# Performance work log

Measured on AMD Instinct MI355X. Metric: run time of the kernel, lower is better.

Reference implementation:

```python
import jax, jax.numpy as jnp
import numpy as np

D_MODEL = 512
NHEAD = 8
DIM = D_MODEL // NHEAD
EPS_ATT = 1e-6
EPS_LN = 1e-5


def layer_norm(x, gamma, beta):
    mu = jnp.mean(x, axis=-1, keepdims=True)
    var = jnp.mean(jnp.square(x - mu), axis=-1, keepdims=True)
    return (x - mu) * jax.lax.rsqrt(var + EPS_LN) * gamma + beta


def setup_inputs() -> dict:
    key = jax.random.key(0)
    ks = jax.random.split(key, 12)
    B, L = 4, 4096
    s = 1.0 / np.sqrt(D_MODEL)
    inp = {
        "q": jax.random.normal(ks[0], (B, L, D_MODEL), jnp.float32),
        "k": jax.random.normal(ks[1], (B, L, D_MODEL), jnp.float32),
        "v": jax.random.normal(ks[2], (B, L, D_MODEL), jnp.float32),
        # weights stored [in, out] so application is x @ W (== torch Linear with W.T)
        "Wq": jax.random.normal(ks[3], (D_MODEL, D_MODEL), jnp.float32) * s,
        "Wk": jax.random.normal(ks[4], (D_MODEL, D_MODEL), jnp.float32) * s,
        "Wv": jax.random.normal(ks[5], (D_MODEL, D_MODEL), jnp.float32) * s,
        "Wm": jax.random.normal(ks[6], (D_MODEL, D_MODEL), jnp.float32) * s,
        "W1": jax.random.normal(ks[7], (D_MODEL, 4 * D_MODEL), jnp.float32) * s,
        "W2": jax.random.normal(ks[8], (4 * D_MODEL, D_MODEL), jnp.float32) * (0.5 * s),
        "g1": jnp.ones((D_MODEL,), jnp.float32),
        "b1": jnp.zeros((D_MODEL,), jnp.float32),
        "g2": jnp.ones((D_MODEL,), jnp.float32),
        "b2": jnp.zeros((D_MODEL,), jnp.float32),
    }
    return inp


def reference(q, k, v, Wq, Wk, Wv, Wm, W1, W2, g1, b1, g2, b2):
    B, L, _ = q.shape
    S = k.shape[1]
    # projections -> [B, L, H, D]
    Qp = (q @ Wq).reshape(B, L, NHEAD, DIM)
    Kp = (k @ Wk).reshape(B, S, NHEAD, DIM)
    Vp = (v @ Wv).reshape(B, S, NHEAD, DIM)
    # elu+1 feature map linear attention
    Q = jax.nn.elu(Qp) + 1.0
    K = jax.nn.elu(Kp) + 1.0
    Vn = Vp / S
    KV = jnp.einsum('nshd,nshv->nhdv', K, Vn)          # [B,H,D,D]
    Z = 1.0 / (jnp.einsum('nlhd,nhd->nlh', Q, K.sum(axis=1)) + EPS_ATT)
    msg = jnp.einsum('nlhd,nhdv,nlh->nlhv', Q, KV, Z) * S  # [B,L,H,D]
    # merge + residual + norm1
    msg = msg.reshape(B, L, D_MODEL) @ Wm
    msg = layer_norm(msg + q, g1, b1)
    # FFN; note original adds mlp output to q (not norm1 output)
    ffn = jax.nn.relu(msg @ W1) @ W2
    out = layer_norm(q + ffn, g2, b2)
    return out
```

## Files before the change

### kernel.cpp

```cpp
#include <hip/hip_runtime.h>

typedef unsigned short u16;
typedef unsigned int u32;

typedef __bf16 bf16x8 __attribute__((ext_vector_type(8)));
typedef float f32x4 __attribute__((ext_vector_type(4)));

#define EPI_BF16 0
#define EPI_ELU1 1
#define EPI_RELU 2
#define EPI_ADDRES_F32 3
#define EPI_PROJ3 4

__device__ __forceinline__ float bf2f(u16 x) {
    u32 u = ((u32)x) << 16;
    return __uint_as_float(u);
}
__device__ __forceinline__ u16 f2bf(float f) {
    u32 u = __float_as_uint(f);
    u32 r = (u + 0x7FFFu + ((u >> 16) & 1u)) >> 16;
    return (u16)r;
}

__device__ __forceinline__ void gload_lds16(const u16* g, u16* l) {
    __builtin_amdgcn_global_load_lds(
        (const __attribute__((address_space(1))) u32*)g,
        (__attribute__((address_space(3))) u32*)l, 16, 0, 0);
}

__global__ __launch_bounds__(256) void prep_k(
    const float* __restrict__ q, const float* __restrict__ k,
    const float* __restrict__ v,
    const float* __restrict__ Wq, const float* __restrict__ Wk,
    const float* __restrict__ Wv, const float* __restrict__ Wm,
    const float* __restrict__ W1, const float* __restrict__ W2,
    u16* __restrict__ qkv_out, u16* __restrict__ wt4_out,
    u16* __restrict__ wt2_out)
{
    int bid = blockIdx.x;
    if (bid < 24576) {
        int w = bid >> 13;
        const float* in = (w == 0) ? q : (w == 1) ? k : v;
        int i = ((bid & 8191) * 256 + threadIdx.x) * 4;
        float4 f = *(const float4*)(in + i);
        ushort4 o;
        o.x = f2bf(f.x); o.y = f2bf(f.y); o.z = f2bf(f.z); o.w = f2bf(f.w);
        *(ushort4*)(qkv_out + (long)w * 8388608 + i) = o;
    } else if (bid < 28672) {
        int idx = (bid - 24576) * 256 + threadIdx.x;
        int w = idx >> 18, local = idx & 262143;
        const float* in = (w == 0) ? Wq : (w == 1) ? Wk : (w == 2) ? Wv : Wm;
        int c = local >> 9, r = local & 511;
        wt4_out[idx] = f2bf(in[r * 512 + c]);
    } else {
        int idx = (bid - 28672) * 256 + threadIdx.x;
        if (idx < 1048576) {
            int c = idx / 512, r = idx % 512;
            wt2_out[idx] = f2bf(W1[(long)r * 2048 + c]);
        } else {
            int local = idx - 1048576;
            int c = local / 2048, r = local % 2048;
            wt2_out[idx] = f2bf(W2[(long)r * 512 + c]);
        }
    }
}

__global__ __launch_bounds__(256) void gemm_bt(
    const u16* __restrict__ A, const u16* __restrict__ Bt,
    void* __restrict__ C, const float* __restrict__ Res,
    int M, int N, int K, int epi)
{
    __shared__ __align__(16) u16 As[2][4096];
    __shared__ __align__(16) u16 Bs[2][4096];

    int t = threadIdx.x;
    int gx = gridDim.x;
    int nwg = gx * gridDim.y;
    int bid = blockIdx.y * gx + blockIdx.x;
    if ((nwg & 7) == 0) {
        int cpx = nwg >> 3;
        bid = (bid & 7) * cpx + (bid >> 3);
    }
    int m0 = (bid / gx) * 128, n0 = (bid % gx) * 128;

    int third = 0;
    if (epi == EPI_PROJ3) {
        third = n0 >> 9;
        A += (long)third * 8388608;
    }

    int wave = t >> 6, lane = t & 63;
    int wm = (wave >> 1) * 64, wn = (wave & 1) * 64;
    int lrow = lane & 15, lk8 = (lane >> 4) * 8;

    f32x4 acc[4][4] = {};

    int srow = wave * 16 + (lane >> 2);
    int scol = (lane & 3) * 8;
    const u16* pA0 = A + (long)(m0 + srow) * K + scol;
    const u16* pB0 = Bt + (long)(n0 + srow) * K + scol;
    const long s64 = (long)64 * K;

    int nt = K >> 5;
    int cur = 0;

    {
        u16* a = As[0] + wave * 512;
        u16* b = Bs[0] + wave * 512;
        gload_lds16(pA0, a);
        gload_lds16(pA0 + s64, a + 2048);
        gload_lds16(pB0, b);
        gload_lds16(pB0 + s64, b + 2048);
    }
    __builtin_amdgcn_s_waitcnt(0);
    __syncthreads();

    for (int kt = 0; kt < nt; ++kt) {
        if (kt + 1 < nt) {
            int k0 = (kt + 1) << 5;
            u16* a = As[cur ^ 1] + wave * 512;
            u16* b = Bs[cur ^ 1] + wave * 512;
            gload_lds16(pA0 + k0, a);
            gload_lds16(pA0 + s64 + k0, a + 2048);
            gload_lds16(pB0 + k0, b);
            gload_lds16(pB0 + s64 + k0, b + 2048);
        }

        const u16* As_c = As[cur];
        const u16* Bs_c = Bs[cur];
        bf16x8 af[4], bfr[4];
#pragma unroll
        for (int mi = 0; mi < 4; mi++)
            af[mi] = *(const bf16x8*)(As_c + (wm + mi * 16 + lrow) * 32 + lk8);
#pragma unroll
        for (int ni = 0; ni < 4; ni++)
            bfr[ni] = *(const bf16x8*)(Bs_c + (wn + ni * 16 + lrow) * 32 + lk8);
#pragma unroll
        for (int mi = 0; mi < 4; mi++)
#pragma unroll
            for (int ni = 0; ni < 4; ni++)
                acc[mi][ni] = __builtin_amdgcn_mfma_f32_16x16x32_bf16(
                    af[mi], bfr[ni], acc[mi][ni], 0, 0, 0);

        if (kt + 1 < nt) {
            __builtin_amdgcn_s_waitcnt(0);
            __syncthreads();
            cur ^= 1;
        }
    }

    int rq = (lane >> 4) * 4;
    int colb = n0 + wn + (lane & 15);
#pragma unroll
    for (int mi = 0; mi < 4; mi++) {
#pragma unroll
        for (int ni = 0; ni < 4; ni++) {
#pragma unroll
            for (int r = 0; r < 4; r++) {
                int row = m0 + wm + mi * 16 + rq + r;
                int col = colb + ni * 16;
                float v0 = acc[mi][ni][r];
                if (epi == EPI_PROJ3) {
                    u16* Cb = (u16*)C + (long)third * 8388608;
                    long idx = (long)row * 512 + (col - (third << 9));
                    float v = (third < 2)
                                  ? (v0 > 0.f ? v0 + 1.f : __expf(v0))
                                  : v0;
                    Cb[idx] = f2bf(v);
                } else {
                    long idx = (long)row * N + col;
                    if (epi == EPI_ELU1) {
                        float v = v0 > 0.f ? v0 + 1.f : __expf(v0);
                        ((u16*)C)[idx] = f2bf(v);
                    } else if (epi == EPI_RELU) {
                        ((u16*)C)[idx] = f2bf(v0 > 0.f ? v0 : 0.f);
                    } else if (epi == EPI_ADDRES_F32) {
                        ((float*)C)[idx] = v0 + Res[idx];
                    } else {
                        ((u16*)C)[idx] = f2bf(v0);
                    }
                }
            }
        }
    }
}

__global__ __launch_bounds__(256) void gemm_bt64(
    const u16* __restrict__ A, const u16* __restrict__ Bt,
    void* __restrict__ C, const float* __restrict__ Res,
    int M, int N, int K, int epi)
{
    __shared__ __align__(16) u16 As[2][8192];
    __shared__ __align__(16) u16 Bs[2][8192];

    int t = threadIdx.x;
    int gx = gridDim.x;
    int nwg = gx * gridDim.y;
    int bid = blockIdx.y * gx + blockIdx.x;
    if ((nwg & 7) == 0) {
        int cpx = nwg >> 3;
        bid = (bid & 7) * cpx + (bid >> 3);
    }
    int m0 = (bid / gx) * 128, n0 = (bid % gx) * 128;

    int wave = t >> 6, lane = t & 63;
    int wm = (wave >> 1) * 64, wn = (wave & 1) * 64;
    int lrow = lane & 15, lk8 = (lane >> 4) * 8;

    f32x4 acc[4][4] = {};

    int srow = wave * 16 + (lane >> 2);
    int scol = (lane & 3) * 8;
    const u16* pA0 = A + (long)(m0 + srow) * K + scol;
    const u16* pB0 = Bt + (long)(n0 + srow) * K + scol;
    const long s64 = (long)64 * K;

    int nt = K >> 6;
    int cur = 0;

    {
        u16* a = As[0] + wave * 512;
        u16* b = Bs[0] + wave * 512;
#pragma unroll
        for (int kk = 0; kk < 2; kk++) {
            gload_lds16(pA0 + kk * 32, a + kk * 4096);
            gload_lds16(pA0 + s64 + kk * 32, a + kk * 4096 + 2048);
            gload_lds16(pB0 + kk * 32, b + kk * 4096);
            gload_lds16(pB0 + s64 + kk * 32, b + kk * 4096 + 2048);
        }
    }
    __builtin_amdgcn_s_waitcnt(0);
    __syncthreads();

    for (int kt = 0; kt < nt; ++kt) {
        if (kt + 1 < nt) {
            int k0 = (kt + 1) << 6;
            u16* a = As[cur ^ 1] + wave * 512;
            u16* b = Bs[cur ^ 1] + wave * 512;
#pragma unroll
            for (int kk = 0; kk < 2; kk++) {
                gload_lds16(pA0 + k0 + kk * 32, a + kk * 4096);
                gload_lds16(pA0 + s64 + k0 + kk * 32, a + kk * 4096 + 2048);
                gload_lds16(pB0 + k0 + kk * 32, b + kk * 4096);
                gload_lds16(pB0 + s64 + k0 + kk * 32, b + kk * 4096 + 2048);
            }
        }

#pragma unroll
        for (int kk = 0; kk < 2; kk++) {
            const u16* As_c = As[cur] + kk * 4096;
            const u16* Bs_c = Bs[cur] + kk * 4096;
            bf16x8 af[4], bfr[4];
#pragma unroll
            for (int mi = 0; mi < 4; mi++)
                af[mi] = *(const bf16x8*)(As_c + (wm + mi * 16 + lrow) * 32 + lk8);
#pragma unroll
            for (int ni = 0; ni < 4; ni++)
                bfr[ni] = *(const bf16x8*)(Bs_c + (wn + ni * 16 + lrow) * 32 + lk8);
#pragma unroll
            for (int mi = 0; mi < 4; mi++)
#pragma unroll
                for (int ni = 0; ni < 4; ni++)
                    acc[mi][ni] = __builtin_amdgcn_mfma_f32_16x16x32_bf16(
                        af[mi], bfr[ni], acc[mi][ni], 0, 0, 0);
        }

        if (kt + 1 < nt) {
            __builtin_amdgcn_s_waitcnt(0);
            __syncthreads();
            cur ^= 1;
        }
    }

    int rq = (lane >> 4) * 4;
    int colb = n0 + wn + (lane & 15);
#pragma unroll
    for (int mi = 0; mi < 4; mi++) {
#pragma unroll
        for (int ni = 0; ni < 4; ni++) {
#pragma unroll
            for (int r = 0; r < 4; r++) {
                int row = m0 + wm + mi * 16 + rq + r;
                int col = colb + ni * 16;
                long idx = (long)row * N + col;
                float v0 = acc[mi][ni][r];
                if (epi == EPI_ELU1) {
                    float v = v0 > 0.f ? v0 + 1.f : __expf(v0);
                    ((u16*)C)[idx] = f2bf(v);
                } else if (epi == EPI_RELU) {
                    ((u16*)C)[idx] = f2bf(v0 > 0.f ? v0 : 0.f);
                } else if (epi == EPI_ADDRES_F32) {
                    ((float*)C)[idx] = v0 + Res[idx];
                } else {
                    ((u16*)C)[idx] = f2bf(v0);
                }
            }
        }
    }
}

__global__ __launch_bounds__(256) void kv_part(
    const u16* __restrict__ Kf, const u16* __restrict__ Vf,
    float* __restrict__ Part, float* __restrict__ KsPart)
{
    __shared__ __align__(16) u16 sKt[64 * 72];
    __shared__ __align__(16) u16 sVt[64 * 72];
    int bh = blockIdx.x;
    int b = bh >> 3, h = bh & 7;
    int t = threadIdx.x;
    int wave = t >> 6, lane = t & 63;
    int dblk = (wave >> 1) * 32, vblk = (wave & 1) * 32;
    int lrow = lane & 15, lk8 = (lane >> 4) * 8;

    f32x4 acc[2][2] = {};
    float ks = 0.f;

    int srow = t >> 2, c16 = (t & 3) * 16;

    for (int st = 0; st < 2; ++st) {
        int s0 = blockIdx.y * 128 + st * 64;
        {
            long g = ((long)b * 4096 + s0 + srow) * 512 + h * 64 + c16;
            uint4 k0 = *(const uint4*)(Kf + g);
            uint4 k1 = *(const uint4*)(Kf + g + 8);
            uint4 v0 = *(const uint4*)(Vf + g);
            uint4 v1 = *(const uint4*)(Vf + g + 8);
            u32 kw[8] = {k0.x, k0.y, k0.z, k0.w, k1.x, k1.y, k1.z, k1.w};
            u32 vw[8] = {v0.x, v0.y, v0.z, v0.w, v1.x, v1.y, v1.z, v1.w};
            if (st) __syncthreads();
#pragma unroll
            for (int j = 0; j < 16; j++) {
                u16 kv_ = (u16)(kw[j >> 1] >> ((j & 1) * 16));
                u16 vv_ = (u16)(vw[j >> 1] >> ((j & 1) * 16));
                sKt[(c16 + j) * 72 + srow] = kv_;
                sVt[(c16 + j) * 72 + srow] = vv_;
            }
        }
        __syncthreads();

#pragma unroll
        for (int ksb = 0; ksb < 2; ++ksb) {
            int ko = ksb * 32 + lk8;
            bf16x8 a0 = *(const bf16x8*)(sKt + (dblk + lrow) * 72 + ko);
            bf16x8 a1 = *(const bf16x8*)(sKt + (dblk + 16 + lrow) * 72 + ko);
            bf16x8 b0 = *(const bf16x8*)(sVt + (vblk + lrow) * 72 + ko);
            bf16x8 b1 = *(const bf16x8*)(sVt + (vblk + 16 + lrow) * 72 + ko);
            acc[0][0] = __builtin_amdgcn_mfma_f32_16x16x32_bf16(a0, b0, acc[0][0], 0, 0, 0);
            acc[0][1] = __builtin_amdgcn_mfma_f32_16x16x32_bf16(a0, b1, acc[0][1], 0, 0, 0);
            acc[1][0] = __builtin_amdgcn_mfma_f32_16x16x32_bf16(a1, b0, acc[1][0], 0, 0, 0);
            acc[1][1] = __builtin_amdgcn_mfma_f32_16x16x32_bf16(a1, b1, acc[1][1], 0, 0, 0);
        }

        if (t < 64) {
            const u32* rowp = (const u32*)(sKt + t * 72);
#pragma unroll
            for (int c = 0; c < 32; c++) {
                u32 w = rowp[c];
                ks += bf2f((u16)w) + bf2f((u16)(w >> 16));
            }
        }
    }

    int rq = (lane >> 4) * 4;
    float* pp = Part + ((long)bh * 32 + blockIdx.y) * 4096;
#pragma unroll
    for (int ti = 0; ti < 2; ti++)
#pragma unroll
        for (int tj = 0; tj < 2; tj++)
#pragma unroll
            for (int r = 0; r < 4; r++) {
                int d = dblk + ti * 16 + rq + r;
                int vcol = vblk + tj * 16 + (lane & 15);
                pp[d * 64 + vcol] = acc[ti][tj][r];
            }
    if (t < 64) KsPart[((bh * 32) + blockIdx.y) * 64 + t] = ks;
}

__global__ __launch_bounds__(256) void kv_reduce(
    const float* __restrict__ Part, const float* __restrict__ KsPart,
    float* __restrict__ KV, float* __restrict__ Ksum)
{
    int i = blockIdx.x * 256 + threadIdx.x;
    if (i < 131072) {
        int bh = i >> 12, dv = i & 4095;
        const float* p = Part + (long)bh * 32 * 4096 + dv;
        float s = 0.f;
#pragma unroll 8
        for (int sp = 0; sp < 32; sp++) s += p[(long)sp * 4096];
        KV[i] = s;
    } else if (i < 133120) {
        int j = i - 131072;
        int bh = j >> 6, d = j & 63;
        const float* p = KsPart + bh * 32 * 64 + d;
        float s = 0.f;
#pragma unroll 8
        for (int sp = 0; sp < 32; sp++) s += p[sp * 64];
        Ksum[j] = s;
    }
}

__global__ __launch_bounds__(256) void msg_k(
    const u16* __restrict__ Q, const float* __restrict__ KV,
    const float* __restrict__ Ksum, u16* __restrict__ Msg)
{
    __shared__ float sKVt[64 * 68];
    __shared__ float sQ[64 * 68];
    __shared__ float sKs[64];
    __shared__ float sZ[64];

    int bh = blockIdx.x;
    int b = bh >> 3, h = bh & 7;
    int l0 = blockIdx.y * 64;
    int t = threadIdx.x, wave = t >> 6, lane = t & 63;

    {
        const float* src = KV + (long)bh * 4096 + t * 16;
        int d = t >> 2;
        int v0 = (t & 3) * 16;
        float4 a0 = *(const float4*)(src);
        float4 a1 = *(const float4*)(src + 4);
        float4 a2 = *(const float4*)(src + 8);
        float4 a3 = *(const float4*)(src + 12);
        float tmp[16] = {a0.x, a0.y, a0.z, a0.w, a1.x, a1.y, a1.z, a1.w,
                         a2.x, a2.y, a2.z, a2.w, a3.x, a3.y, a3.z, a3.w};
#pragma unroll
        for (int j = 0; j < 16; j++) sKVt[(v0 + j) * 68 + d] = tmp[j];
    }
    {
        int row = t >> 2, c = (t & 3) * 16;
        const u16* src = Q + ((long)b * 4096 + l0 + row) * 512 + h * 64 + c;
        uint4 q0 = *(const uint4*)(src);
        uint4 q1 = *(const uint4*)(src + 8);
        float* dq = sQ + row * 68 + c;
        u32 qw[8] = {q0.x, q0.y, q0.z, q0.w, q1.x, q1.y, q1.z, q1.w};
#pragma unroll
        for (int j = 0; j < 8; j++) {
            dq[2 * j]     = __uint_as_float(qw[j] << 16);
            dq[2 * j + 1] = __uint_as_float(qw[j] & 0xFFFF0000u);
        }
    }
    if (t < 64) sKs[t] = Ksum[bh * 64 + t];
    __syncthreads();

    float kv[64];
    {
        const float* kr = sKVt + lane * 68;
#pragma unroll
        for (int j = 0; j < 16; j++) {
            float4 x = *(const float4*)(kr + 4 * j);
            kv[4 * j]     = x.x; kv[4 * j + 1] = x.y;
            kv[4 * j + 2] = x.z; kv[4 * j + 3] = x.w;
        }
    }
    if (t < 64) {
        const float* qr = sQ + t * 68;
        float zp = 0.f;
#pragma unroll
        for (int d = 0; d < 64; d++) zp += qr[d] * sKs[d];
        sZ[t] = 1.f / (zp + 1e-6f);
    }
    __syncthreads();

    const long obase = ((long)b * 4096 + l0) * 512 + h * 64 + lane;
    int lbase = wave * 16;
#pragma unroll 4
    for (int i = 0; i < 16; i++) {
        int ll = lbase + i;
        const float* qr = sQ + ll * 68;
        float a0 = 0.f, a1 = 0.f, a2 = 0.f, a3 = 0.f;
#pragma unroll
        for (int db = 0; db < 16; db++) {
            float4 q4 = *(const float4*)(qr + 4 * db);
            a0 += q4.x * kv[4 * db];
            a1 += q4.y * kv[4 * db + 1];
            a2 += q4.z * kv[4 * db + 2];
            a3 += q4.w * kv[4 * db + 3];
        }
        float acc = (a0 + a1) + (a2 + a3);
        Msg[obase + (long)ll * 512] = f2bf(acc * sZ[ll]);
    }
}

__global__ __launch_bounds__(256) void ln_k(
    const float* __restrict__ X, const float* __restrict__ g,
    const float* __restrict__ bta, u16* __restrict__ OutB,
    float* __restrict__ OutF, int out_f32)
{
    int wave = threadIdx.x >> 6, lane = threadIdx.x & 63;
    long row = (long)blockIdx.x * 4 + wave;
    const float* x = X + row * 512 + lane * 8;
    float4 a = *(const float4*)(x);
    float4 c = *(const float4*)(x + 4);
    float s = (a.x + a.y) + (a.z + a.w) + (c.x + c.y) + (c.z + c.w);
    float sq = a.x * a.x + a.y * a.y + a.z * a.z + a.w * a.w +
               c.x * c.x + c.y * c.y + c.z * c.z + c.w * c.w;
#pragma unroll
    for (int off = 32; off > 0; off >>= 1) {
        s += __shfl_xor(s, off, 64);
        sq += __shfl_xor(sq, off, 64);
    }
    float mu = s * (1.f / 512.f);
    float var = sq * (1.f / 512.f) - mu * mu;
    float rstd = rsqrtf(var + 1e-5f);
    float4 g0 = *(const float4*)(g + lane * 8);
    float4 g1 = *(const float4*)(g + lane * 8 + 4);
    float4 b0 = *(const float4*)(bta + lane * 8);
    float4 b1 = *(const float4*)(bta + lane * 8 + 4);
    float y0 = (a.x - mu) * rstd * g0.x + b0.x;
    float y1 = (a.y - mu) * rstd * g0.y + b0.y;
    float y2 = (a.z - mu) * rstd * g0.z + b0.z;
    float y3 = (a.w - mu) * rstd * g0.w + b0.w;
    float y4 = (c.x - mu) * rstd * g1.x + b1.x;
    float y5 = (c.y - mu) * rstd * g1.y + b1.y;
    float y6 = (c.z - mu) * rstd * g1.z + b1.z;
    float y7 = (c.w - mu) * rstd * g1.w + b1.w;
    if (out_f32) {
        float* o = OutF + row * 512 + lane * 8;
        *(float4*)(o) = make_float4(y0, y1, y2, y3);
        *(float4*)(o + 4) = make_float4(y4, y5, y6, y7);
    } else {
        u32 w0 = (u32)f2bf(y0) | ((u32)f2bf(y1) << 16);
        u32 w1 = (u32)f2bf(y2) | ((u32)f2bf(y3) << 16);
        u32 w2 = (u32)f2bf(y4) | ((u32)f2bf(y5) << 16);
        u32 w3 = (u32)f2bf(y6) | ((u32)f2bf(y7) << 16);
        uint4 o = {w0, w1, w2, w3};
        *(uint4*)(OutB + row * 512 + lane * 8) = o;
    }
}

extern "C" void kernel_launch(void* const* d_in, const int* in_sizes, int n_in,
                              void* d_out, int out_size, void* d_ws, size_t ws_size,
                              hipStream_t stream) {
    const float* q  = (const float*)d_in[0];
    const float* k  = (const float*)d_in[1];
    const float* v  = (const float*)d_in[2];
    const float* Wq = (const float*)d_in[3];
    const float* Wk = (const float*)d_in[4];
    const float* Wv = (const float*)d_in[5];
    const float* Wm = (const float*)d_in[6];
    const float* W1 = (const float*)d_in[7];
    const float* W2 = (const float*)d_in[8];
    const float* g1 = (const float*)d_in[9];
    const float* b1 = (const float*)d_in[10];
    const float* g2 = (const float*)d_in[11];
    const float* b2 = (const float*)d_in[12];

    char* ws = (char*)d_ws;
    u16* WTq = (u16*)(ws + 0);
    u16* W1T = (u16*)(ws + 2097152);
    u16* qc  = (u16*)(ws + 6291456);
    u16* Qb  = (u16*)(ws + 56623104);
    u16* Kb  = (u16*)(ws + 73400320);
    u16* Vb  = (u16*)(ws + 90177536);
    float* KVb = (float*)(ws + 106954752);
    float* KSb = (float*)(ws + 107479040);
    u16* Msg = (u16*)(ws + 107487232);
    float* Part = (float*)(ws + 23068672);
    float* KsPart = (float*)(ws + 6291456);
    float* xpre = (float*)(ws + 23068672);
    u16* x1  = qc;
    u16* Hid = (u16*)(ws + 56623104);

    prep_k<<<dim3(36864), 256, 0, stream>>>(q, k, v, Wq, Wk, Wv, Wm, W1, W2,
                                            qc, WTq, W1T);

    gemm_bt<<<dim3(12, 128), 256, 0, stream>>>(qc, WTq, Qb, nullptr, 16384, 1536, 512, EPI_PROJ3);

    kv_part<<<dim3(32, 32), 256, 0, stream>>>(Kb, Vb, Part, KsPart);
    kv_reduce<<<dim3(520), 256, 0, stream>>>(Part, KsPart, KVb, KSb);
    msg_k<<<dim3(32, 64), 256, 0, stream>>>(Qb, KVb, KSb, Msg);

    gemm_bt64<<<dim3(4, 128), 256, 0, stream>>>(Msg, (u16*)(ws + 1572864), xpre, q, 16384, 512, 512, EPI_ADDRES_F32);
    ln_k<<<dim3(4096), 256, 0, stream>>>(xpre, g1, b1, x1, nullptr, 0);

    gemm_bt64<<<dim3(16, 128), 256, 0, stream>>>(x1, W1T, Hid, nullptr, 16384, 2048, 512, EPI_RELU);
    gemm_bt64<<<dim3(4, 128), 256, 0, stream>>>(Hid, (u16*)(ws + 4194304), xpre, q, 16384, 512, 2048, EPI_ADDRES_F32);
    ln_k<<<dim3(4096), 256, 0, stream>>>(xpre, g2, b2, nullptr, (float*)d_out, 1);
}
```

Before: 443.2 us.

## Fuse fp32-to-bf16 input conversion into projection GEMM; use MFMA for message

The projection GEMM now reads fp32 q/k/v directly, converts them to bf16 in registers and stores them to LDS, so prep_k no longer makes a separate conversion pass over the activations. The KV reduction now writes transposed KV as a bf16 hi/lo split pair. The message kernel then computes Q·KV with two MFMA passes instead of scalar fp32 FMAs. This removes a large read/write round trip and the scalar inner loop, at the cost of register-staged A loads in the GEMM and extra MFMAs to keep near-fp32 accuracy for KV.

```diff
diff --git a/kernel.cpp b/kernel.cpp
--- a/kernel.cpp
+++ b/kernel.cpp
@@ -10,7 +10,6 @@
 #define EPI_ELU1 1
 #define EPI_RELU 2
 #define EPI_ADDRES_F32 3
-#define EPI_PROJ3 4
 
 __device__ __forceinline__ float bf2f(u16 x) {
     u32 u = ((u32)x) << 16;
@@ -21,6 +20,9 @@
     u32 r = (u + 0x7FFFu + ((u >> 16) & 1u)) >> 16;
     return (u16)r;
 }
+__device__ __forceinline__ u32 pack2(float a, float b) {
+    return (u32)f2bf(a) | ((u32)f2bf(b) << 16);
+}
 
 __device__ __forceinline__ void gload_lds16(const u16* g, u16* l) {
     __builtin_amdgcn_global_load_lds(
@@ -29,31 +31,20 @@
 }
 
 __global__ __launch_bounds__(256) void prep_k(
-    const float* __restrict__ q, const float* __restrict__ k,
-    const float* __restrict__ v,
     const float* __restrict__ Wq, const float* __restrict__ Wk,
     const float* __restrict__ Wv, const float* __restrict__ Wm,
     const float* __restrict__ W1, const float* __restrict__ W2,
-    u16* __restrict__ qkv_out, u16* __restrict__ wt4_out,
-    u16* __restrict__ wt2_out)
+    u16* __restrict__ wt4_out, u16* __restrict__ wt2_out)
 {
     int bid = blockIdx.x;
-    if (bid < 24576) {
-        int w = bid >> 13;
-        const float* in = (w == 0) ? q : (w == 1) ? k : v;
-        int i = ((bid & 8191) * 256 + threadIdx.x) * 4;
-        float4 f = *(const float4*)(in + i);
-        ushort4 o;
-        o.x = f2bf(f.x); o.y = f2bf(f.y); o.z = f2bf(f.z); o.w = f2bf(f.w);
-        *(ushort4*)(qkv_out + (long)w * 8388608 + i) = o;
-    } else if (bid < 28672) {
-        int idx = (bid - 24576) * 256 + threadIdx.x;
+    if (bid < 4096) {
+        int idx = bid * 256 + threadIdx.x;
         int w = idx >> 18, local = idx & 262143;
         const float* in = (w == 0) ? Wq : (w == 1) ? Wk : (w == 2) ? Wv : Wm;
         int c = local >> 9, r = local & 511;
         wt4_out[idx] = f2bf(in[r * 512 + c]);
     } else {
-        int idx = (bid - 28672) * 256 + threadIdx.x;
+        int idx = (bid - 4096) * 256 + threadIdx.x;
         if (idx < 1048576) {
             int c = idx / 512, r = idx % 512;
             wt2_out[idx] = f2bf(W1[(long)r * 2048 + c]);
@@ -65,10 +56,10 @@
     }
 }
 
-__global__ __launch_bounds__(256) void gemm_bt(
-    const u16* __restrict__ A, const u16* __restrict__ Bt,
-    void* __restrict__ C, const float* __restrict__ Res,
-    int M, int N, int K, int epi)
+__global__ __launch_bounds__(256) void gemm_proj3(
+    const float* __restrict__ Aq, const float* __restrict__ Ak,
+    const float* __restrict__ Av, const u16* __restrict__ Bt,
+    u16* __restrict__ C)
 {
     __shared__ __align__(16) u16 As[2][4096];
     __shared__ __align__(16) u16 Bs[2][4096];
@@ -77,17 +68,13 @@
     int gx = gridDim.x;
     int nwg = gx * gridDim.y;
     int bid = blockIdx.y * gx + blockIdx.x;
-    if ((nwg & 7) == 0) {
+    {
         int cpx = nwg >> 3;
         bid = (bid & 7) * cpx + (bid >> 3);
     }
     int m0 = (bid / gx) * 128, n0 = (bid % gx) * 128;
-
-    int third = 0;
-    if (epi == EPI_PROJ3) {
-        third = n0 >> 9;
-        A += (long)third * 8388608;
-    }
+    int third = n0 >> 9;
+    const float* Af = (third == 0) ? Aq : (third == 1) ? Ak : Av;
 
     int wave = t >> 6, lane = t & 63;
     int wm = (wave >> 1) * 64, wn = (wave & 1) * 64;
@@ -97,33 +84,44 @@
 
     int srow = wave * 16 + (lane >> 2);
     int scol = (lane & 3) * 8;
-    const u16* pA0 = A + (long)(m0 + srow) * K + scol;
-    const u16* pB0 = Bt + (long)(n0 + srow) * K + scol;
-    const long s64 = (long)64 * K;
-
-    int nt = K >> 5;
+    const float* pAf = Af + (long)(m0 + srow) * 512 + scol;
+    const u16* pB0 = Bt + (long)(n0 + srow) * 512 + scol;
+    const long s64 = (long)64 * 512;
+    u16* myA0 = (u16*)As[0];
+    u16* myA1 = (u16*)As[1];
+    int wslot = wave * 512 + lane * 8;
+
+    int nt = 16;
     int cur = 0;
 
     {
-        u16* a = As[0] + wave * 512;
-        u16* b = Bs[0] + wave * 512;
-        gload_lds16(pA0, a);
-        gload_lds16(pA0 + s64, a + 2048);
-        gload_lds16(pB0, b);
-        gload_lds16(pB0 + s64, b + 2048);
+        float4 a0 = *(const float4*)(pAf);
+        float4 a1 = *(const float4*)(pAf + 4);
+        float4 a2 = *(const float4*)(pAf + s64);
+        float4 a3 = *(const float4*)(pAf + s64 + 4);
+        gload_lds16(pB0, Bs[0] + wave * 512);
+        gload_lds16(pB0 + s64, Bs[0] + wave * 512 + 2048);
+        uint4 w0 = {pack2(a0.x, a0.y), pack2(a0.z, a0.w),
+                    pack2(a1.x, a1.y), pack2(a1.z, a1.w)};
+        uint4 w1 = {pack2(a2.x, a2.y), pack2(a2.z, a2.w),
+                    pack2(a3.x, a3.y), pack2(a3.z, a3.w)};
+        *(uint4*)(myA0 + wslot) = w0;
+        *(uint4*)(myA0 + wslot + 2048) = w1;
     }
     __builtin_amdgcn_s_waitcnt(0);
     __syncthreads();
 
     for (int kt = 0; kt < nt; ++kt) {
+        float4 a0, a1, a2, a3;
         if (kt + 1 < nt) {
             int k0 = (kt + 1) << 5;
-            u16* a = As[cur ^ 1] + wave * 512;
             u16* b = Bs[cur ^ 1] + wave * 512;
-            gload_lds16(pA0 + k0, a);
-            gload_lds16(pA0 + s64 + k0, a + 2048);
             gload_lds16(pB0 + k0, b);
             gload_lds16(pB0 + s64 + k0, b + 2048);
+            a0 = *(const float4*)(pAf + k0);
+            a1 = *(const float4*)(pAf + k0 + 4);
+            a2 = *(const float4*)(pAf + s64 + k0);
+            a3 = *(const float4*)(pAf + s64 + k0 + 4);
         }
 
         const u16* As_c = As[cur];
@@ -144,6 +142,13 @@
 
         if (kt + 1 < nt) {
             __builtin_amdgcn_s_waitcnt(0);
+            u16* dst = (cur == 0) ? myA1 : myA0;
+            uint4 w0 = {pack2(a0.x, a0.y), pack2(a0.z, a0.w),
+                        pack2(a1.x, a1.y), pack2(a1.z, a1.w)};
+            uint4 w1 = {pack2(a2.x, a2.y), pack2(a2.z, a2.w),
+                        pack2(a3.x, a3.y), pack2(a3.z, a3.w)};
+            *(uint4*)(dst + wslot) = w0;
+            *(uint4*)(dst + wslot + 2048) = w1;
             __syncthreads();
             cur ^= 1;
         }
@@ -151,6 +156,7 @@
 
     int rq = (lane >> 4) * 4;
     int colb = n0 + wn + (lane & 15);
+    u16* Cb = C + (long)third * 8388608;
 #pragma unroll
     for (int mi = 0; mi < 4; mi++) {
 #pragma unroll
@@ -158,28 +164,12 @@
 #pragma unroll
             for (int r = 0; r < 4; r++) {
                 int row = m0 + wm + mi * 16 + rq + r;
-                int col = colb + ni * 16;
+                int col = colb + ni * 16 - (third << 9);
                 float v0 = acc[mi][ni][r];
-                if (epi == EPI_PROJ3) {
-                    u16* Cb = (u16*)C + (long)third * 8388608;
-                    long idx = (long)row * 512 + (col - (third << 9));
-                    float v = (third < 2)
-                                  ? (v0 > 0.f ? v0 + 1.f : __expf(v0))
-                                  : v0;
-                    Cb[idx] = f2bf(v);
-                } else {
-                    long idx = (long)row * N + col;
-                    if (epi == EPI_ELU1) {
-                        float v = v0 > 0.f ? v0 + 1.f : __expf(v0);
-                        ((u16*)C)[idx] = f2bf(v);
-                    } else if (epi == EPI_RELU) {
-                        ((u16*)C)[idx] = f2bf(v0 > 0.f ? v0 : 0.f);
-                    } else if (epi == EPI_ADDRES_F32) {
-                        ((float*)C)[idx] = v0 + Res[idx];
-                    } else {
-                        ((u16*)C)[idx] = f2bf(v0);
-                    }
-                }
+                float v = (third < 2)
+                              ? (v0 > 0.f ? v0 + 1.f : __expf(v0))
+                              : v0;
+                Cb[(long)row * 512 + col] = f2bf(v);
             }
         }
     }
@@ -378,16 +368,22 @@
 
 __global__ __launch_bounds__(256) void kv_reduce(
     const float* __restrict__ Part, const float* __restrict__ KsPart,
-    float* __restrict__ KV, float* __restrict__ Ksum)
+    u16* __restrict__ KVthi, u16* __restrict__ KVtlo,
+    float* __restrict__ Ksum)
 {
     int i = blockIdx.x * 256 + threadIdx.x;
     if (i < 131072) {
         int bh = i >> 12, dv = i & 4095;
+        int d = dv >> 6, v = dv & 63;
         const float* p = Part + (long)bh * 32 * 4096 + dv;
         float s = 0.f;
 #pragma unroll 8
         for (int sp = 0; sp < 32; sp++) s += p[(long)sp * 4096];
-        KV[i] = s;
+        u16 hi = f2bf(s);
+        u16 lo = f2bf(s - bf2f(hi));
+        long o = (long)bh * 4096 + v * 64 + d;
+        KVthi[o] = hi;
+        KVtlo[o] = lo;
     } else if (i < 133120) {
         int j = i - 131072;
         int bh = j >> 6, d = j & 63;
@@ -400,11 +396,13 @@
 }
 
 __global__ __launch_bounds__(256) void msg_k(
-    const u16* __restrict__ Q, const float* __restrict__ KV,
-    const float* __restrict__ Ksum, u16* __restrict__ Msg)
-{
-    __shared__ float sKVt[64 * 68];
-    __shared__ float sQ[64 * 68];
+    const u16* __restrict__ Q, const u16* __restrict__ KVthi,
+    const u16* __restrict__ KVtlo, const float* __restrict__ Ksum,
+    u16* __restrict__ Msg)
+{
+    __shared__ __align__(16) u16 sQ[64 * 72];
+    __shared__ __align__(16) u16 sHi[64 * 72];
+    __shared__ __align__(16) u16 sLo[64 * 72];
     __shared__ float sKs[64];
     __shared__ float sZ[64];
 
@@ -413,71 +411,59 @@
     int l0 = blockIdx.y * 64;
     int t = threadIdx.x, wave = t >> 6, lane = t & 63;
 
-    {
-        const float* src = KV + (long)bh * 4096 + t * 16;
-        int d = t >> 2;
-        int v0 = (t & 3) * 16;
-        float4 a0 = *(const float4*)(src);
-        float4 a1 = *(const float4*)(src + 4);
-        float4 a2 = *(const float4*)(src + 8);
-        float4 a3 = *(const float4*)(src + 12);
-        float tmp[16] = {a0.x, a0.y, a0.z, a0.w, a1.x, a1.y, a1.z, a1.w,
-                         a2.x, a2.y, a2.z, a2.w, a3.x, a3.y, a3.z, a3.w};
-#pragma unroll
-        for (int j = 0; j < 16; j++) sKVt[(v0 + j) * 68 + d] = tmp[j];
-    }
-    {
-        int row = t >> 2, c = (t & 3) * 16;
-        const u16* src = Q + ((long)b * 4096 + l0 + row) * 512 + h * 64 + c;
-        uint4 q0 = *(const uint4*)(src);
-        uint4 q1 = *(const uint4*)(src + 8);
-        float* dq = sQ + row * 68 + c;
-        u32 qw[8] = {q0.x, q0.y, q0.z, q0.w, q1.x, q1.y, q1.z, q1.w};
-#pragma unroll
-        for (int j = 0; j < 8; j++) {
-            dq[2 * j]     = __uint_as_float(qw[j] << 16);
-            dq[2 * j + 1] = __uint_as_float(qw[j] & 0xFFFF0000u);
-        }
+#pragma unroll
+    for (int p = 0; p < 2; ++p) {
+        int c = t + p * 256;
+        int row = c >> 3, cc = c & 7;
+        int dsto = row * 72 + cc * 8;
+        uint4 qv = *(const uint4*)(Q + ((long)b * 4096 + l0 + row) * 512 +
+                                   h * 64 + cc * 8);
+        uint4 hv = *(const uint4*)(KVthi + (long)bh * 4096 + c * 8);
+        uint4 lv = *(const uint4*)(KVtlo + (long)bh * 4096 + c * 8);
+        *(uint4*)(sQ + dsto) = qv;
+        *(uint4*)(sHi + dsto) = hv;
+        *(uint4*)(sLo + dsto) = lv;
     }
     if (t < 64) sKs[t] = Ksum[bh * 64 + t];
     __syncthreads();
 
-    float kv[64];
-    {
-        const float* kr = sKVt + lane * 68;
-#pragma unroll
-        for (int j = 0; j < 16; j++) {
-            float4 x = *(const float4*)(kr + 4 * j);
-            kv[4 * j]     = x.x; kv[4 * j + 1] = x.y;
-            kv[4 * j + 2] = x.z; kv[4 * j + 3] = x.w;
-        }
-    }
     if (t < 64) {
-        const float* qr = sQ + t * 68;
         float zp = 0.f;
 #pragma unroll
-        for (int d = 0; d < 64; d++) zp += qr[d] * sKs[d];
+        for (int d = 0; d < 64; d++) zp += bf2f(sQ[t * 72 + d]) * sKs[d];
         sZ[t] = 1.f / (zp + 1e-6f);
     }
+
+    int lrow = lane & 15, lk8 = (lane >> 4) * 8;
+    bf16x8 af[2];
+#pragma unroll
+    for (int ksb = 0; ksb < 2; ksb++)
+        af[ksb] = *(const bf16x8*)(sQ + (wave * 16 + lrow) * 72 + ksb * 32 + lk8);
+
+    f32x4 acc[4] = {};
+#pragma unroll
+    for (int vt = 0; vt < 4; vt++) {
+#pragma unroll
+        for (int ksb = 0; ksb < 2; ksb++) {
+            int bo = (vt * 16 + lrow) * 72 + ksb * 32 + lk8;
+            bf16x8 bh_ = *(const bf16x8*)(sHi + bo);
+            bf16x8 bl_ = *(const bf16x8*)(sLo + bo);
+            acc[vt] = __builtin_amdgcn_mfma_f32_16x16x32_bf16(af[ksb], bh_, acc[vt], 0, 0, 0);
+            acc[vt] = __builtin_amdgcn_mfma_f32_16x16x32_bf16(af[ksb], bl_, acc[vt], 0, 0, 0);
+        }
+    }
     __syncthreads();
 
-    const long obase = ((long)b * 4096 + l0) * 512 + h * 64 + lane;
-    int lbase = wave * 16;
-#pragma unroll 4
-    for (int i = 0; i < 16; i++) {
-        int ll = lbase + i;
-        const float* qr = sQ + ll * 68;
-        float a0 = 0.f, a1 = 0.f, a2 = 0.f, a3 = 0.f;
-#pragma unroll
-        for (int db = 0; db < 16; db++) {
-            float4 q4 = *(const float4*)(qr + 4 * db);
-            a0 += q4.x * kv[4 * db];
-            a1 += q4.y * kv[4 * db + 1];
-            a2 += q4.z * kv[4 * db + 2];
-            a3 += q4.w * kv[4 * db + 3];
-        }
-        float acc = (a0 + a1) + (a2 + a3);
-        Msg[obase + (long)ll * 512] = f2bf(acc * sZ[ll]);
+    int rq = (lane >> 4) * 4;
+#pragma unroll
+    for (int vt = 0; vt < 4; vt++) {
+#pragma unroll
+        for (int r = 0; r < 4; r++) {
+            int ll = wave * 16 + rq + r;
+            int v = vt * 16 + (lane & 15);
+            float out = acc[vt][r] * sZ[ll];
+            Msg[((long)b * 4096 + l0 + ll) * 512 + h * 64 + v] = f2bf(out);
+        }
     }
 }
 
@@ -548,27 +534,26 @@
     char* ws = (char*)d_ws;
     u16* WTq = (u16*)(ws + 0);
     u16* W1T = (u16*)(ws + 2097152);
-    u16* qc  = (u16*)(ws + 6291456);
     u16* Qb  = (u16*)(ws + 56623104);
     u16* Kb  = (u16*)(ws + 73400320);
     u16* Vb  = (u16*)(ws + 90177536);
-    float* KVb = (float*)(ws + 106954752);
+    u16* KVthi = (u16*)(ws + 106954752);
+    u16* KVtlo = (u16*)(ws + 107216896);
     float* KSb = (float*)(ws + 107479040);
     u16* Msg = (u16*)(ws + 107487232);
     float* Part = (float*)(ws + 23068672);
     float* KsPart = (float*)(ws + 6291456);
     float* xpre = (float*)(ws + 23068672);
-    u16* x1  = qc;
+    u16* x1  = (u16*)(ws + 6291456);
     u16* Hid = (u16*)(ws + 56623104);
 
-    prep_k<<<dim3(36864), 256, 0, stream>>>(q, k, v, Wq, Wk, Wv, Wm, W1, W2,
-                                            qc, WTq, W1T);
-
-    gemm_bt<<<dim3(12, 128), 256, 0, stream>>>(qc, WTq, Qb, nullptr, 16384, 1536, 512, EPI_PROJ3);
+    prep_k<<<dim3(12288), 256, 0, stream>>>(Wq, Wk, Wv, Wm, W1, W2, WTq, W1T);
+
+    gemm_proj3<<<dim3(12, 128), 256, 0, stream>>>(q, k, v, WTq, Qb);
 
     kv_part<<<dim3(32, 32), 256, 0, stream>>>(Kb, Vb, Part, KsPart);
-    kv_reduce<<<dim3(520), 256, 0, stream>>>(Part, KsPart, KVb, KSb);
-    msg_k<<<dim3(32, 64), 256, 0, stream>>>(Qb, KVb, KSb, Msg);
+    kv_reduce<<<dim3(520), 256, 0, stream>>>(Part, KsPart, KVthi, KVtlo, KSb);
+    msg_k<<<dim3(32, 64), 256, 0, stream>>>(Qb, KVthi, KVtlo, KSb, Msg);
 
     gemm_bt64<<<dim3(4, 128), 256, 0, stream>>>(Msg, (u16*)(ws + 1572864), xpre, q, 16384, 512, 512, EPI_ADDRES_F32);
     ln_k<<<dim3(4096), 256, 0, stream>>>(xpre, g1, b1, x1, nullptr, 0);
```

Result: faster. 421.6 us (-4.9%).
